# Kernel optimization log

Hardware: AMD Instinct MI355X
Metric: run time of the kernel (lower is better)

Reference implementation:

```python
import jax, jax.numpy as jnp
import numpy as np

B, N, E = 4, 4096, 65536
HID, F_N, F_E, ROUNDS = 128, 32, 16, 3


def setup_inputs() -> dict:
    key = jax.random.key(0)
    ks = jax.random.split(key, 32)
    p = lambda k, shape: 0.02 * jax.random.normal(k, shape, dtype=jnp.float32)
    inp = {
        "nodes": jax.random.normal(ks[0], (B, N, F_N), dtype=jnp.float32),
        "edge_feat": jax.random.normal(ks[1], (B, E, F_E), dtype=jnp.float32),
        "edges": jax.random.randint(ks[2], (B, E, 2), 0, N).astype(jnp.int64),
        "node_mask": jnp.ones((B, N), dtype=bool),
        "edge_mask": jnp.ones((B, E), dtype=bool),
        # projections (stored as (in, out))
        "W_node": p(ks[3], (F_N, HID)),
        "W_edge": p(ks[4], (F_E, HID)),
        "marker": p(ks[5], (HID,)),
        # per-round MLP weights, stacked on leading rounds dim
        "eW1": p(ks[6], (ROUNDS, 3 * HID, HID)),
        "eb1": jnp.zeros((ROUNDS, HID), jnp.float32),
        "eW2": p(ks[7], (ROUNDS, HID, HID)),
        "eb2": jnp.zeros((ROUNDS, HID), jnp.float32),
        "nW1": p(ks[8], (ROUNDS, 2 * HID, HID)),
        "nb1": jnp.zeros((ROUNDS, HID), jnp.float32),
        "nW2": p(ks[9], (ROUNDS, HID, HID)),
        "nb2": jnp.zeros((ROUNDS, HID), jnp.float32),
    }
    return inp


def reference(nodes, edge_feat, edges, node_mask, edge_mask,
              W_node, W_edge, marker, eW1, eb1, eW2, eb2, nW1, nb1, nW2, nb2):
    b, n, _ = nodes.shape
    h = nodes @ W_node                       # (B,N,H)
    ef = edge_feat @ W_edge                  # (B,E,H)
    src = jnp.clip(edges[..., 0], 0, n - 1)  # (B,E)
    dst = jnp.clip(edges[..., 1], 0, n - 1)
    bidx = jnp.arange(b)[:, None]            # (B,1) for batched gather/scatter
    em = edge_mask.astype(h.dtype)[..., None]
    nm = node_mask.astype(h.dtype)[..., None]
    for r in range(ROUNDS):
        h_src = h[bidx, src]                 # (B,E,H) gather
        h_dst = h[bidx, dst]
        cat = jnp.concatenate([h_src, h_dst, ef], axis=-1)   # (B,E,3H)
        msg = jax.nn.silu(cat @ eW1[r] + eb1[r]) @ eW2[r] + eb2[r]
        msg = msg * em
        agg = jnp.zeros_like(h).at[bidx, dst].add(msg)       # scatter-add to nodes
        cat_node = jnp.concatenate([h, agg], axis=-1)        # (B,N,2H)
        upd = jax.nn.silu(cat_node @ nW1[r] + nb1[r]) @ nW2[r] + nb2[r]
        h = (h + upd) * nm
    marker_tok = jnp.broadcast_to(marker[None, None, :], (b, 1, HID))
    return jnp.concatenate([marker_tok, h], axis=1)          # (B,1+N,H)
```

## Files before the change

### kernel.cpp

```cpp
#include <hip/hip_runtime.h>
#include <hip/hip_bf16.h>
#include <cstdint>
#include <cstddef>

#define BB 4
#define NN 4096
#define EE 65536
#define HID 128
#define FN 32
#define FE 16
#define NROUNDS 3

#define XP 168
#define XNP 264
#define PP 136
#define YPITCH 136

typedef __attribute__((ext_vector_type(8))) short short8;
typedef __attribute__((ext_vector_type(4))) float f32x4;
typedef unsigned int uint_t;

__device__ __forceinline__ size_t hrow(int b, int n) {
    return ((size_t)b * (NN + 1) + 1 + n) * HID;
}

__device__ __forceinline__ short f2bf(float f) {
    __hip_bfloat16 h = __float2bfloat16(f);
    return *reinterpret_cast<short*>(&h);
}

__device__ __forceinline__ float bf2f(short s) {
    union { uint32_t u; float f; } v;
    v.u = ((uint32_t)(unsigned short)s) << 16;
    return v.f;
}

__device__ __forceinline__ float silu(float x) {
    return x * __builtin_amdgcn_rcpf(1.0f + __expf(-x));
}

__device__ __forceinline__ int clipn(int x) {
    return x < 0 ? 0 : (x > NN - 1 ? NN - 1 : x);
}

__global__ void proj_nodes_kernel(const float* __restrict__ nodes,
                                  const float* __restrict__ Wn,
                                  float* __restrict__ hbuf,
                                  short* __restrict__ hbf,
                                  const float* __restrict__ marker,
                                  const float* __restrict__ We,
                                  const float* __restrict__ eW1,
                                  float* __restrict__ Wec,
                                  uint_t* __restrict__ cnt) {
    __shared__ float nd[8][FN];
    int t = threadIdx.x;
    int row0 = blockIdx.x * 8;

    if (blockIdx.x < 4) {
        hbuf[((size_t)blockIdx.x * (NN + 1)) * HID + t] = marker[t];
    } else if (blockIdx.x < 68) {
        int base = (blockIdx.x - 4) * 256 + t * 2;
        cnt[base] = 0u; cnt[base + 1] = 0u;
    } else if (blockIdx.x < 116) {
        int lb = blockIdx.x - 68; int r = lb >> 4; int i = lb & 15;
        const float* w1 = eW1 + ((size_t)r * 384 + 256) * HID;
        float acc = 0.f;
        for (int k = 0; k < HID; ++k)
            acc += We[i * HID + k] * w1[k * HID + t];
        Wec[((size_t)r * 16 + i) * HID + t] = acc;
    }

    for (int i = 0; i < 2; ++i) {
        int idx = i * 128 + t; int r = idx >> 5; int c = idx & 31;
        nd[r][c] = nodes[(size_t)(row0 + r) * FN + c];
    }
    __syncthreads();
    float acc[8] = {0.f,0.f,0.f,0.f,0.f,0.f,0.f,0.f};
    #pragma unroll
    for (int k = 0; k < FN; ++k) {
        float w = Wn[k * HID + t];
        #pragma unroll
        for (int r = 0; r < 8; ++r) acc[r] += nd[r][k] * w;
    }
    #pragma unroll
    for (int r = 0; r < 8; ++r) {
        int row = row0 + r; int b = row >> 12; int n = row & (NN - 1);
        hbuf[hrow(b, n) + t] = acc[r];
        hbf[(size_t)row * HID + t] = f2bf(acc[r]);
    }
}

__device__ __forceinline__ void pack_generic(const float* __restrict__ W,
                                             short* __restrict__ P,
                                             int KT, size_t rstrideW,
                                             int lb, int lane) {
    int nt = lb & 7;
    int kt = (lb >> 3) % KT;
    int r  = lb / (8 * KT);
    const float* Wr = W + (size_t)r * rstrideW;
    int n  = nt * 16 + (lane & 15);
    int k0 = kt * 32 + (lane >> 4) * 8;
    short v[8];
    #pragma unroll
    for (int i = 0; i < 8; ++i) v[i] = f2bf(Wr[(size_t)(k0 + i) * HID + n]);
    size_t idx = (((size_t)(r * KT + kt) * 8 + nt) * 64 + lane) * 8;
    *(uint4*)&P[idx] = *(uint4*)v;
}

__global__ void pack_all_kernel(const float* __restrict__ eW1,
                                const float* __restrict__ Wec,
                                const float* __restrict__ eW2,
                                const float* __restrict__ nW1,
                                const float* __restrict__ nW2,
                                short* __restrict__ W1p,
                                short* __restrict__ W2p,
                                short* __restrict__ eYp,
                                short* __restrict__ nW1p,
                                short* __restrict__ nW2p) {
    int lane = threadIdx.x;
    int bid = blockIdx.x;
    if (bid < 120) {
        const int KT = 5;
        int nt = bid & 7; int kt = (bid >> 3) % KT; int r = bid / (8 * KT);
        int n  = nt * 16 + (lane & 15);
        int k0 = kt * 32 + (lane >> 4) * 8;
        short v[8];
        #pragma unroll
        for (int i = 0; i < 8; ++i) {
            int k = k0 + i;
            float x;
            if (k < 128)      x = eW1[((size_t)r * 384 + k) * HID + n];
            else if (k < 144) x = Wec[((size_t)r * 16 + (k - 128)) * HID + n];
            else              x = 0.f;
            v[i] = f2bf(x);
        }
        size_t idx = (((size_t)(r * KT + kt) * 8 + nt) * 64 + lane) * 8;
        *(uint4*)&W1p[idx] = *(uint4*)v;
    } else if (bid < 216) {
        pack_generic(eW2, W2p, 4, (size_t)HID * HID, bid - 120, lane);
    } else if (bid < 312) {
        pack_generic(eW1 + (size_t)128 * HID, eYp, 4, (size_t)384 * HID,
                     bid - 216, lane);
    } else if (bid < 504) {
        pack_generic(nW1, nW1p, 8, (size_t)2 * HID * HID, bid - 312, lane);
    } else {
        pack_generic(nW2, nW2p, 4, (size_t)HID * HID, bid - 504, lane);
    }
}

__global__ void hist_kernel(const int* __restrict__ edges,
                            uint_t* __restrict__ cnt) {
    int i = blockIdx.x * 256 + threadIdx.x;
    int b = i >> 16;
    int d = clipn(edges[(size_t)i * 2 + 1]);
    atomicAdd(&cnt[b * NN + d], 1u);
}

__global__ void scan_kernel(const uint_t* __restrict__ cnt,
                            uint_t* __restrict__ cursor) {
    __shared__ uint_t ps[256];
    int t = threadIdx.x;
    int base = t * 64;
    uint_t s = 0;
    for (int i = 0; i < 64; ++i) s += cnt[base + i];
    ps[t] = s;
    __syncthreads();
    for (int off = 1; off < 256; off <<= 1) {
        uint_t v = (t >= off) ? ps[t - off] : 0u;
        __syncthreads();
        ps[t] += v;
        __syncthreads();
    }
    uint_t run = ps[t] - s;
    for (int i = 0; i < 64; ++i) {
        cursor[base + i] = run;
        run += cnt[base + i];
    }
}

__global__ void scatter_kernel(const int* __restrict__ edges,
                               uint_t* __restrict__ cursor,
                               uint_t* __restrict__ eidx) {
    int i = blockIdx.x * 256 + threadIdx.x;
    int b = i >> 16;
    int d = clipn(edges[(size_t)i * 2 + 1]);
    uint_t p = atomicAdd(&cursor[b * NN + d], 1u);
    eidx[p] = (uint_t)(i & (EE - 1));
}

__global__ void permute_kernel(const int* __restrict__ edges,
                               const int* __restrict__ emask,
                               const float* __restrict__ edge_feat,
                               const uint_t* __restrict__ eidx,
                               uint_t* __restrict__ meta,
                               short* __restrict__ efs) {
    int p = blockIdx.x * 256 + threadIdx.x;
    int b = p >> 16;
    int e = (int)eidx[p];
    int2 pr = *(const int2*)&edges[((size_t)b * EE + e) * 2];
    int s = clipn(pr.x), d = clipn(pr.y);
    uint_t mk = emask[(size_t)b * EE + e] ? 1u : 0u;
    meta[p] = (uint_t)s | ((uint_t)d << 12) | (mk << 24);
    const float* src = edge_feat + ((size_t)b * EE + e) * FE;
    short v[16];
    #pragma unroll
    for (int i = 0; i < 16; ++i) v[i] = f2bf(src[i]);
    *(uint4*)(efs + (size_t)p * FE)     = *(uint4*)v;
    *(uint4*)(efs + (size_t)p * FE + 8) = *(uint4*)(v + 8);
}

__global__ __launch_bounds__(256, 6)
void proj_y_kernel(const short* __restrict__ hbf,
                   const short* __restrict__ Wp,
                   const float* __restrict__ b1,
                   short* __restrict__ Y,
                   float* __restrict__ agg) {
    __shared__ short X[16 * YPITCH];
    int t = threadIdx.x;
    int row0 = blockIdx.x * 16;

    #pragma unroll
    for (int i = 0; i < 2; ++i) {
        int c = i * 256 + t;
        *(float4*)(agg + (size_t)row0 * HID + c * 4) =
            make_float4(0.f, 0.f, 0.f, 0.f);
    }

    {
        int e = t >> 4; int s = t & 15;
        uint4 v = *(const uint4*)(hbf + (size_t)(row0 + e) * HID + s * 8);
        *(uint4*)((char*)X + e * (YPITCH * 2) + s * 16) = v;
    }
    __syncthreads();

    int lane = t & 63;
    int w    = t >> 6;
    int n0 = w * 32;
    int lr = lane & 15;
    int lg = lane >> 4;

    f32x4 acc[2];
    #pragma unroll
    for (int nf = 0; nf < 2; ++nf) {
        float bv = b1[n0 + nf * 16 + lr];
        acc[nf] = (f32x4){bv, bv, bv, bv};
    }
    const char* Xb = (const char*)X;
    for (int kt = 0; kt < 4; ++kt) {
        short8 a = *(const short8*)(Xb + lr * (YPITCH * 2)
                                       + (kt * 32 + lg * 8) * 2);
        const short* wp = Wp + (((size_t)kt * 8 + (n0 >> 4)) * 64 + lane) * 8;
        #pragma unroll
        for (int nf = 0; nf < 2; ++nf) {
            short8 bf = *(const short8*)(wp + (size_t)nf * 64 * 8);
            acc[nf] = __builtin_amdgcn_mfma_f32_16x16x32_bf16(a, bf, acc[nf], 0, 0, 0);
        }
    }
    #pragma unroll
    for (int r = 0; r < 4; ++r) {
        int row = lg * 4 + r;
        #pragma unroll
        for (int nf = 0; nf < 2; ++nf)
            Y[(size_t)(row0 + row) * HID + n0 + nf * 16 + lr]
                = f2bf(acc[nf][r]);
    }
}

__global__ __launch_bounds__(256, 6)
void edge_mfma_csr_kernel(const short* __restrict__ hbf,
                          const short* __restrict__ efs,
                          const uint_t* __restrict__ meta,
                          const short* __restrict__ Y,
                          const short* __restrict__ W1p,
                          const short* __restrict__ W2p,
                          const float* __restrict__ b2,
                          float* __restrict__ agg) {
    __shared__ short X[64 * XP];
    __shared__ int sdst[64];
    __shared__ float smf[64];
    short* Pl = X;

    int t = threadIdx.x;
    int p0 = blockIdx.x * 64;
    int b  = p0 >> 16;

    if (t < 64) {
        uint_t m = meta[p0 + t];
        sdst[t] = (int)((m >> 12) & 0xFFFu);
        smf[t]  = (m >> 24) ? 1.f : 0.f;
    }
    __syncthreads();

    #pragma unroll
    for (int i = 0; i < 4; ++i) {
        int c = i * 256 + t; int e = c >> 4; int s = c & 15;
        int src = (int)(meta[p0 + e] & 0xFFFu);
        uint4 v = *(const uint4*)(hbf + ((size_t)b * NN + src) * HID + s * 8);
        *(uint4*)((char*)X + e * (XP * 2) + s * 16) = v;
    }
    if (t < 128) {
        int e = t >> 1; int s = t & 1;
        uint4 v = *(const uint4*)(efs + (size_t)(p0 + e) * FE + s * 8);
        *(uint4*)((char*)X + e * (XP * 2) + 256 + s * 16) = v;
    }
    if (t < 128) {
        int e = t >> 1; int s = t & 1;
        *(uint4*)((char*)X + e * (XP * 2) + 288 + s * 16) = make_uint4(0,0,0,0);
    }

    int lane = t & 63;
    int w    = t >> 6;
    int m0 = (w & 1) * 32;
    int n0 = (w >> 1) * 64;
    int lr = lane & 15;
    int lg = lane >> 4;

    f32x4 acc[2][4];
    #pragma unroll
    for (int mf = 0; mf < 2; ++mf)
        #pragma unroll
        for (int r = 0; r < 4; ++r) {
            int row = m0 + mf * 16 + lg * 4 + r;
            const short* yp = Y + ((size_t)b * NN + sdst[row]) * HID + n0 + lr;
            #pragma unroll
            for (int nf = 0; nf < 4; ++nf)
                acc[mf][nf][r] = bf2f(yp[nf * 16]);
        }
    __syncthreads();

    const char* Xb = (const char*)X;
    for (int kt = 0; kt < 5; ++kt) {
        short8 a[2];
        #pragma unroll
        for (int mf = 0; mf < 2; ++mf)
            a[mf] = *(const short8*)(Xb + (m0 + mf * 16 + lr) * (XP * 2)
                                        + (kt * 32 + lg * 8) * 2);
        const short* wp = W1p + (((size_t)kt * 8 + (n0 >> 4)) * 64 + lane) * 8;
        #pragma unroll
        for (int nf = 0; nf < 4; ++nf) {
            short8 bf = *(const short8*)(wp + (size_t)nf * 64 * 8);
            #pragma unroll
            for (int mf = 0; mf < 2; ++mf)
                acc[mf][nf] = __builtin_amdgcn_mfma_f32_16x16x32_bf16(
                    a[mf], bf, acc[mf][nf], 0, 0, 0);
        }
    }
    __syncthreads();

    #pragma unroll
    for (int mf = 0; mf < 2; ++mf)
        #pragma unroll
        for (int nf = 0; nf < 4; ++nf)
            #pragma unroll
            for (int r = 0; r < 4; ++r) {
                int row = m0 + mf * 16 + lg * 4 + r;
                int col = n0 + nf * 16 + lr;
                Pl[row * PP + col] = f2bf(silu(acc[mf][nf][r]));
            }
    __syncthreads();

    f32x4 acc2[2][4];
    #pragma unroll
    for (int nf = 0; nf < 4; ++nf) {
        float bv = b2[n0 + nf * 16 + lr];
        #pragma unroll
        for (int mf = 0; mf < 2; ++mf)
            acc2[mf][nf] = (f32x4){bv, bv, bv, bv};
    }
    const char* Pb = (const char*)Pl;
    for (int kt = 0; kt < 4; ++kt) {
        short8 a[2];
        #pragma unroll
        for (int mf = 0; mf < 2; ++mf)
            a[mf] = *(const short8*)(Pb + (m0 + mf * 16 + lr) * (PP * 2)
                                        + (kt * 32 + lg * 8) * 2);
        const short* wp = W2p + (((size_t)kt * 8 + (n0 >> 4)) * 64 + lane) * 8;
        #pragma unroll
        for (int nf = 0; nf < 4; ++nf) {
            short8 bf = *(const short8*)(wp + (size_t)nf * 64 * 8);
            #pragma unroll
            for (int mf = 0; mf < 2; ++mf)
                acc2[mf][nf] = __builtin_amdgcn_mfma_f32_16x16x32_bf16(
                    a[mf], bf, acc2[mf][nf], 0, 0, 0);
        }
    }
    __syncthreads();

    #pragma unroll
    for (int mf = 0; mf < 2; ++mf)
        #pragma unroll
        for (int r = 0; r < 4; ++r) {
            int row = m0 + mf * 16 + lg * 4 + r;
            float m = smf[row];
            #pragma unroll
            for (int nf = 0; nf < 4; ++nf)
                Pl[row * PP + n0 + nf * 16 + lr] = f2bf(acc2[mf][nf][r] * m);
        }
    __syncthreads();

    {
        int half = t >> 7;
        int c    = t & 127;
        int r0 = half * 32, r1 = r0 + 32;
        float run = 0.f;
        int cur = sdst[r0];
        for (int r = r0; r < r1; ++r) {
            int d = sdst[r];
            if (d != cur) {
                atomicAdd(&agg[((size_t)b * NN + cur) * HID + c], run);
                run = 0.f; cur = d;
            }
            run += bf2f(Pl[r * PP + c]);
        }
        atomicAdd(&agg[((size_t)b * NN + cur) * HID + c], run);
    }
}

__global__ __launch_bounds__(256, 6)
void node_mfma_kernel(const short* __restrict__ hbf_in,
                      const float* __restrict__ agg,
                      const int* __restrict__ nmask,
                      const short* __restrict__ W1p,
                      const short* __restrict__ W2p,
                      const float* __restrict__ b1,
                      const float* __restrict__ b2,
                      float* __restrict__ hout,
                      short* __restrict__ hbf_out) {
    __shared__ short X[16 * XNP];
    __shared__ int smk[16];
    short* Pl = X;

    int t = threadIdx.x;
    int row0 = blockIdx.x * 16;
    int b  = row0 >> 12;
    int nn0 = row0 & (NN - 1);

    if (t < 16) smk[t] = nmask[row0 + t];

    {
        int e = t >> 4; int s = t & 15;
        uint4 v = *(const uint4*)(hbf_in + (size_t)(row0 + e) * HID + s * 8);
        *(uint4*)((char*)X + e * (XNP * 2) + s * 16) = v;
    }
    #pragma unroll
    for (int i = 0; i < 2; ++i) {
        int c = i * 256 + t; int e = c >> 5; int s = c & 31;
        float4 f = *(const float4*)(agg + (size_t)(row0 + e) * HID + s * 4);
        short v[4] = { f2bf(f.x), f2bf(f.y), f2bf(f.z), f2bf(f.w) };
        *(uint2*)((char*)X + e * (XNP * 2) + 256 + s * 8) = *(uint2*)v;
    }
    __syncthreads();

    int lane = t & 63;
    int w    = t >> 6;
    int n0 = w * 32;
    int lr = lane & 15;
    int lg = lane >> 4;

    f32x4 acc[2];
    #pragma unroll
    for (int nf = 0; nf < 2; ++nf) {
        float bv = b1[n0 + nf * 16 + lr];
        acc[nf] = (f32x4){bv, bv, bv, bv};
    }
    const char* Xb = (const char*)X;
    for (int kt = 0; kt < 8; ++kt) {
        short8 a = *(const short8*)(Xb + lr * (XNP * 2)
                                       + (kt * 32 + lg * 8) * 2);
        const short* wp = W1p + (((size_t)kt * 8 + (n0 >> 4)) * 64 + lane) * 8;
        #pragma unroll
        for (int nf = 0; nf < 2; ++nf) {
            short8 bf = *(const short8*)(wp + (size_t)nf * 64 * 8);
            acc[nf] = __builtin_amdgcn_mfma_f32_16x16x32_bf16(a, bf, acc[nf], 0, 0, 0);
        }
    }
    __syncthreads();

    #pragma unroll
    for (int nf = 0; nf < 2; ++nf)
        #pragma unroll
        for (int r = 0; r < 4; ++r) {
            int row = lg * 4 + r;
            int col = n0 + nf * 16 + lr;
            Pl[row * PP + col] = f2bf(silu(acc[nf][r]));
        }
    __syncthreads();

    f32x4 acc2[2];
    #pragma unroll
    for (int nf = 0; nf < 2; ++nf) {
        float bv = b2[n0 + nf * 16 + lr];
        acc2[nf] = (f32x4){bv, bv, bv, bv};
    }
    const char* Pb = (const char*)Pl;
    for (int kt = 0; kt < 4; ++kt) {
        short8 a = *(const short8*)(Pb + lr * (PP * 2)
                                       + (kt * 32 + lg * 8) * 2);
        const short* wp = W2p + (((size_t)kt * 8 + (n0 >> 4)) * 64 + lane) * 8;
        #pragma unroll
        for (int nf = 0; nf < 2; ++nf) {
            short8 bf = *(const short8*)(wp + (size_t)nf * 64 * 8);
            acc2[nf] = __builtin_amdgcn_mfma_f32_16x16x32_bf16(a, bf, acc2[nf], 0, 0, 0);
        }
    }

    #pragma unroll
    for (int r = 0; r < 4; ++r) {
        int rl = lg * 4 + r;
        float m = smk[rl] ? 1.f : 0.f;
        size_t ho = hrow(b, nn0 + rl);
        size_t hb = (size_t)(row0 + rl) * HID;
        #pragma unroll
        for (int nf = 0; nf < 2; ++nf) {
            int col = n0 + nf * 16 + lr;
            float hold = hout[ho + col];
            float hn = (hold + acc2[nf][r]) * m;
            hout[ho + col] = hn;
            hbf_out[hb + col] = f2bf(hn);
        }
    }
}

extern "C" void kernel_launch(void* const* d_in, const int* in_sizes, int n_in,
                              void* d_out, int out_size, void* d_ws, size_t ws_size,
                              hipStream_t stream) {
    const float* nodes     = (const float*)d_in[0];
    const float* edge_feat = (const float*)d_in[1];
    const int*   edges     = (const int*)d_in[2];
    const int*   node_mask = (const int*)d_in[3];
    const int*   edge_mask = (const int*)d_in[4];
    const float* W_node    = (const float*)d_in[5];
    const float* W_edge    = (const float*)d_in[6];
    const float* marker    = (const float*)d_in[7];
    const float* eW1       = (const float*)d_in[8];
    const float* eb1       = (const float*)d_in[9];
    const float* eW2       = (const float*)d_in[10];
    const float* eb2       = (const float*)d_in[11];
    const float* nW1       = (const float*)d_in[12];
    const float* nb1       = (const float*)d_in[13];
    const float* nW2       = (const float*)d_in[14];
    const float* nb2       = (const float*)d_in[15];
    float* out = (float*)d_out;

    const size_t HN = (size_t)BB * NN * HID;
    char* wsb = (char*)d_ws;
    float*  agg    = (float*)wsb;   wsb += HN * 4;
    short*  hbf    = (short*)wsb;   wsb += HN * 2;
    short*  Yb     = (short*)wsb;   wsb += HN * 2;
    float*  Wec    = (float*)wsb;   wsb += 3 * 16 * HID * 4;
    short*  W1p    = (short*)wsb;   wsb += 3 * 5 * 4096 * 2;
    short*  W2p    = (short*)wsb;   wsb += 3 * 4 * 4096 * 2;
    short*  eYp    = (short*)wsb;   wsb += 3 * 4 * 4096 * 2;
    short*  nW1p   = (short*)wsb;   wsb += 3 * 8 * 4096 * 2;
    short*  nW2p   = (short*)wsb;   wsb += 3 * 4 * 4096 * 2;
    uint_t* cnt    = (uint_t*)wsb;  wsb += (size_t)BB * NN * 4;
    uint_t* cursor = (uint_t*)wsb;  wsb += (size_t)BB * NN * 4;
    uint_t* eidx   = (uint_t*)wsb;  wsb += (size_t)BB * EE * 4;
    uint_t* meta   = (uint_t*)wsb;  wsb += (size_t)BB * EE * 4;
    short*  efs    = (short*)wsb;   wsb += (size_t)BB * EE * FE * 2;
    if ((size_t)(wsb - (char*)d_ws) > ws_size) return;

    proj_nodes_kernel<<<(BB * NN) / 8, 128, 0, stream>>>(
        nodes, W_node, out, hbf, marker, W_edge, eW1, Wec, cnt);
    pack_all_kernel<<<600, 64, 0, stream>>>(
        eW1, Wec, eW2, nW1, nW2, W1p, W2p, eYp, nW1p, nW2p);
    hist_kernel<<<(BB * EE) / 256, 256, 0, stream>>>(edges, cnt);
    scan_kernel<<<1, 256, 0, stream>>>(cnt, cursor);
    scatter_kernel<<<(BB * EE) / 256, 256, 0, stream>>>(edges, cursor, eidx);
    permute_kernel<<<(BB * EE) / 256, 256, 0, stream>>>(
        edges, edge_mask, edge_feat, eidx, meta, efs);

    for (int r = 0; r < NROUNDS; ++r) {
        proj_y_kernel<<<(BB * NN) / 16, 256, 0, stream>>>(
            hbf, eYp + (size_t)r * 4 * 4096, eb1 + r * HID, Yb, agg);
        edge_mfma_csr_kernel<<<(BB * EE) / 64, 256, 0, stream>>>(
            hbf, efs, meta, Yb,
            W1p + (size_t)r * 5 * 4096,
            W2p + (size_t)r * 4 * 4096,
            eb2 + r * HID,
            agg);
        node_mfma_kernel<<<(BB * NN) / 16, 256, 0, stream>>>(
            hbf, agg, node_mask,
            nW1p + (size_t)r * 8 * 4096,
            nW2p + (size_t)r * 4 * 4096,
            nb1 + r * HID,
            nb2 + r * HID,
            out, hbf);
    }
}
```

Before: 239.5 us.

## Fuse edge sort permute, fold next-round Y projection into node kernel, segment-parallel scatter

Merges the scatter and permute kernels so edge metadata and bf16 edge features are written straight to their sorted slot, which removes the eidx buffer and one pass over the edges. The next round's Y projection and the agg zeroing move into the tail of the node kernel, so the per-round proj_y launch is gone. The edge kernel finds destination segments with a ballot and gives each (segment, column) pair its own thread for the scatter-add, where before two threads per column walked 32 rows each. The scan now reads and writes uint4 vectors. The cost is that edge order inside a destination is set by atomic order, and the node kernel gets longer and uses more registers.

```diff
diff --git a/kernel.cpp b/kernel.cpp
--- a/kernel.cpp
+++ b/kernel.cpp
@@ -152,7 +152,8 @@
                             uint_t* __restrict__ cnt) {
     int i = blockIdx.x * 256 + threadIdx.x;
     int b = i >> 16;
-    int d = clipn(edges[(size_t)i * 2 + 1]);
+    int2 pr = *(const int2*)&edges[(size_t)i * 2];
+    int d = clipn(pr.y);
     atomicAdd(&cnt[b * NN + d], 1u);
 }
 
@@ -160,51 +161,53 @@
                             uint_t* __restrict__ cursor) {
     __shared__ uint_t ps[256];
     int t = threadIdx.x;
-    int base = t * 64;
+    const uint4* c4 = (const uint4*)cnt + (size_t)t * 16;
+    uint4 v[16];
     uint_t s = 0;
-    for (int i = 0; i < 64; ++i) s += cnt[base + i];
+    #pragma unroll
+    for (int i = 0; i < 16; ++i) {
+        v[i] = c4[i];
+        s += v[i].x + v[i].y + v[i].z + v[i].w;
+    }
     ps[t] = s;
     __syncthreads();
     for (int off = 1; off < 256; off <<= 1) {
-        uint_t v = (t >= off) ? ps[t - off] : 0u;
+        uint_t x = (t >= off) ? ps[t - off] : 0u;
         __syncthreads();
-        ps[t] += v;
+        ps[t] += x;
         __syncthreads();
     }
     uint_t run = ps[t] - s;
-    for (int i = 0; i < 64; ++i) {
-        cursor[base + i] = run;
-        run += cnt[base + i];
-    }
-}
-
-__global__ void scatter_kernel(const int* __restrict__ edges,
-                               uint_t* __restrict__ cursor,
-                               uint_t* __restrict__ eidx) {
+    uint4* o4 = (uint4*)cursor + (size_t)t * 16;
+    #pragma unroll
+    for (int i = 0; i < 16; ++i) {
+        uint4 o;
+        o.x = run;
+        o.y = o.x + v[i].x;
+        o.z = o.y + v[i].y;
+        o.w = o.z + v[i].z;
+        run = o.w + v[i].w;
+        o4[i] = o;
+    }
+}
+
+__global__ void scatter_permute_kernel(const int* __restrict__ edges,
+                                       const int* __restrict__ emask,
+                                       const float* __restrict__ edge_feat,
+                                       uint_t* __restrict__ cursor,
+                                       uint_t* __restrict__ meta,
+                                       short* __restrict__ efs) {
     int i = blockIdx.x * 256 + threadIdx.x;
     int b = i >> 16;
-    int d = clipn(edges[(size_t)i * 2 + 1]);
+    int2 pr = *(const int2*)&edges[(size_t)i * 2];
+    int s = clipn(pr.x), d = clipn(pr.y);
+    uint_t mk = emask[i] ? 1u : 0u;
     uint_t p = atomicAdd(&cursor[b * NN + d], 1u);
-    eidx[p] = (uint_t)(i & (EE - 1));
-}
-
-__global__ void permute_kernel(const int* __restrict__ edges,
-                               const int* __restrict__ emask,
-                               const float* __restrict__ edge_feat,
-                               const uint_t* __restrict__ eidx,
-                               uint_t* __restrict__ meta,
-                               short* __restrict__ efs) {
-    int p = blockIdx.x * 256 + threadIdx.x;
-    int b = p >> 16;
-    int e = (int)eidx[p];
-    int2 pr = *(const int2*)&edges[((size_t)b * EE + e) * 2];
-    int s = clipn(pr.x), d = clipn(pr.y);
-    uint_t mk = emask[(size_t)b * EE + e] ? 1u : 0u;
     meta[p] = (uint_t)s | ((uint_t)d << 12) | (mk << 24);
-    const float* src = edge_feat + ((size_t)b * EE + e) * FE;
+    const float* src = edge_feat + (size_t)i * FE;
     short v[16];
     #pragma unroll
-    for (int i = 0; i < 16; ++i) v[i] = f2bf(src[i]);
+    for (int k = 0; k < 16; ++k) v[k] = f2bf(src[k]);
     *(uint4*)(efs + (size_t)p * FE)     = *(uint4*)v;
     *(uint4*)(efs + (size_t)p * FE + 8) = *(uint4*)(v + 8);
 }
@@ -225,7 +228,6 @@
         *(float4*)(agg + (size_t)row0 * HID + c * 4) =
             make_float4(0.f, 0.f, 0.f, 0.f);
     }
-
     {
         int e = t >> 4; int s = t & 15;
         uint4 v = *(const uint4*)(hbf + (size_t)(row0 + e) * HID + s * 8);
@@ -278,6 +280,8 @@
     __shared__ short X[64 * XP];
     __shared__ int sdst[64];
     __shared__ float smf[64];
+    __shared__ unsigned short segs[65];
+    __shared__ int nseg;
     short* Pl = X;
 
     int t = threadIdx.x;
@@ -288,6 +292,16 @@
         uint_t m = meta[p0 + t];
         sdst[t] = (int)((m >> 12) & 0xFFFu);
         smf[t]  = (m >> 24) ? 1.f : 0.f;
+        uint_t pm = __shfl_up(m, 1);
+        int flag = (t == 0) || (((m ^ pm) & 0x00FFF000u) != 0u);
+        unsigned long long mask = __ballot(flag);
+        int rank = __popcll(mask & ((1ull << t) - 1ull));
+        if (flag) segs[rank] = (unsigned short)t;
+        if (t == 0) {
+            int ns = __popcll(mask);
+            nseg = ns;
+            segs[ns] = 64;
+        }
     }
     __syncthreads();
 
@@ -302,9 +316,6 @@
         int e = t >> 1; int s = t & 1;
         uint4 v = *(const uint4*)(efs + (size_t)(p0 + e) * FE + s * 8);
         *(uint4*)((char*)X + e * (XP * 2) + 256 + s * 16) = v;
-    }
-    if (t < 128) {
-        int e = t >> 1; int s = t & 1;
         *(uint4*)((char*)X + e * (XP * 2) + 288 + s * 16) = make_uint4(0,0,0,0);
     }
 
@@ -399,20 +410,16 @@
     __syncthreads();
 
     {
-        int half = t >> 7;
-        int c    = t & 127;
-        int r0 = half * 32, r1 = r0 + 32;
-        float run = 0.f;
-        int cur = sdst[r0];
-        for (int r = r0; r < r1; ++r) {
-            int d = sdst[r];
-            if (d != cur) {
-                atomicAdd(&agg[((size_t)b * NN + cur) * HID + c], run);
-                run = 0.f; cur = d;
-            }
-            run += bf2f(Pl[r * PP + c]);
-        }
-        atomicAdd(&agg[((size_t)b * NN + cur) * HID + c], run);
+        int ns = nseg;
+        for (int task = t; task < (ns << 7); task += 256) {
+            int s = task >> 7;
+            int c = task & 127;
+            int r0 = segs[s], r1 = segs[s + 1];
+            float run = 0.f;
+            for (int r = r0; r < r1; ++r)
+                run += bf2f(Pl[r * PP + c]);
+            atomicAdd(&agg[((size_t)b * NN + sdst[r0]) * HID + c], run);
+        }
     }
 }
 
@@ -425,7 +432,11 @@
                       const float* __restrict__ b1,
                       const float* __restrict__ b2,
                       float* __restrict__ hout,
-                      short* __restrict__ hbf_out) {
+                      short* __restrict__ hbf_out,
+                      short* __restrict__ Ynext,
+                      const short* __restrict__ eYpN,
+                      const float* __restrict__ b1N,
+                      float* __restrict__ aggz) {
     __shared__ short X[16 * XNP];
     __shared__ int smk[16];
     short* Pl = X;
@@ -504,6 +515,7 @@
         }
     }
 
+    short hn_bf[2][4];
     #pragma unroll
     for (int r = 0; r < 4; ++r) {
         int rl = lg * 4 + r;
@@ -516,8 +528,53 @@
             float hold = hout[ho + col];
             float hn = (hold + acc2[nf][r]) * m;
             hout[ho + col] = hn;
-            hbf_out[hb + col] = f2bf(hn);
-        }
+            short hb16 = f2bf(hn);
+            hbf_out[hb + col] = hb16;
+            hn_bf[nf][r] = hb16;
+        }
+    }
+
+    if (Ynext == nullptr) return;
+
+    __syncthreads();
+    #pragma unroll
+    for (int r = 0; r < 4; ++r) {
+        int row = lg * 4 + r;
+        #pragma unroll
+        for (int nf = 0; nf < 2; ++nf)
+            Pl[row * PP + n0 + nf * 16 + lr] = hn_bf[nf][r];
+    }
+    __syncthreads();
+
+    f32x4 accy[2];
+    #pragma unroll
+    for (int nf = 0; nf < 2; ++nf) {
+        float bv = b1N[n0 + nf * 16 + lr];
+        accy[nf] = (f32x4){bv, bv, bv, bv};
+    }
+    for (int kt = 0; kt < 4; ++kt) {
+        short8 a = *(const short8*)((const char*)Pl + lr * (PP * 2)
+                                       + (kt * 32 + lg * 8) * 2);
+        const short* wp = eYpN + (((size_t)kt * 8 + (n0 >> 4)) * 64 + lane) * 8;
+        #pragma unroll
+        for (int nf = 0; nf < 2; ++nf) {
+            short8 bf = *(const short8*)(wp + (size_t)nf * 64 * 8);
+            accy[nf] = __builtin_amdgcn_mfma_f32_16x16x32_bf16(a, bf, accy[nf], 0, 0, 0);
+        }
+    }
+    #pragma unroll
+    for (int r = 0; r < 4; ++r) {
+        int row = lg * 4 + r;
+        #pragma unroll
+        for (int nf = 0; nf < 2; ++nf)
+            Ynext[(size_t)(row0 + row) * HID + n0 + nf * 16 + lr]
+                = f2bf(accy[nf][r]);
+    }
+    #pragma unroll
+    for (int i = 0; i < 2; ++i) {
+        int c = i * 256 + t;
+        *(float4*)(aggz + (size_t)row0 * HID + c * 4) =
+            make_float4(0.f, 0.f, 0.f, 0.f);
     }
 }
 
@@ -555,7 +612,6 @@
     short*  nW2p   = (short*)wsb;   wsb += 3 * 4 * 4096 * 2;
     uint_t* cnt    = (uint_t*)wsb;  wsb += (size_t)BB * NN * 4;
     uint_t* cursor = (uint_t*)wsb;  wsb += (size_t)BB * NN * 4;
-    uint_t* eidx   = (uint_t*)wsb;  wsb += (size_t)BB * EE * 4;
     uint_t* meta   = (uint_t*)wsb;  wsb += (size_t)BB * EE * 4;
     short*  efs    = (short*)wsb;   wsb += (size_t)BB * EE * FE * 2;
     if ((size_t)(wsb - (char*)d_ws) > ws_size) return;
@@ -566,25 +622,30 @@
         eW1, Wec, eW2, nW1, nW2, W1p, W2p, eYp, nW1p, nW2p);
     hist_kernel<<<(BB * EE) / 256, 256, 0, stream>>>(edges, cnt);
     scan_kernel<<<1, 256, 0, stream>>>(cnt, cursor);
-    scatter_kernel<<<(BB * EE) / 256, 256, 0, stream>>>(edges, cursor, eidx);
-    permute_kernel<<<(BB * EE) / 256, 256, 0, stream>>>(
-        edges, edge_mask, edge_feat, eidx, meta, efs);
+    scatter_permute_kernel<<<(BB * EE) / 256, 256, 0, stream>>>(
+        edges, edge_mask, edge_feat, cursor, meta, efs);
+
+    proj_y_kernel<<<(BB * NN) / 16, 256, 0, stream>>>(
+        hbf, eYp, eb1, Yb, agg);
 
     for (int r = 0; r < NROUNDS; ++r) {
-        proj_y_kernel<<<(BB * NN) / 16, 256, 0, stream>>>(
-            hbf, eYp + (size_t)r * 4 * 4096, eb1 + r * HID, Yb, agg);
         edge_mfma_csr_kernel<<<(BB * EE) / 64, 256, 0, stream>>>(
             hbf, efs, meta, Yb,
             W1p + (size_t)r * 5 * 4096,
             W2p + (size_t)r * 4 * 4096,
             eb2 + r * HID,
             agg);
+        bool last = (r == NROUNDS - 1);
         node_mfma_kernel<<<(BB * NN) / 16, 256, 0, stream>>>(
             hbf, agg, node_mask,
             nW1p + (size_t)r * 8 * 4096,
             nW2p + (size_t)r * 4 * 4096,
             nb1 + r * HID,
             nb2 + r * HID,
-            out, hbf);
-    }
-}
+            out, hbf,
+            last ? nullptr : Yb,
+            last ? eYp : eYp + (size_t)(r + 1) * 4 * 4096,
+            last ? eb1 : eb1 + (size_t)(r + 1) * HID,
+            agg);
+    }
+}
```

After: 220.1 us. -8.1%, faster.
